# Performance work log

Hardware: AMD Instinct MI355X
Metric: run time of the kernel (lower is better)

Reference implementation:

```python
import jax, jax.numpy as jnp
import numpy as np

H = 0.01      # RK4 step size (parameter.h)
LAM = 1.0     # stage-cost gate penalty
R_COST = 0.1  # scalar control cost R
WMIN, WMAX = -0.01, 0.01  # disturbance range
B, N_STATES, T_STEPS = 8192, 2, 2048

# substituted plant dynamics (parameter.x1_dot / parameter.x2_dot)
def _x1_dot(x1, x2, u):
    return -2.0 * x1 + x2 + u

def _x2_dot(x1, x2, u):
    return x1 - 2.0 * x2 + u

def _rk4_step(x, u):
    # Faithful to RungeKutta.f: k2 == k3 (both evaluated at x2 + h/2)
    x1, x2 = x[0], x[1]
    k1 = jnp.stack([_x1_dot(x1, x2, u), _x2_dot(x1, x2, u)])
    k2 = jnp.stack([_x1_dot(x1, x2 + H / 2, u), _x2_dot(x1, x2 + H / 2, u)])
    k4 = jnp.stack([_x1_dot(x1, x2 + H, u), _x2_dot(x1, x2 + H, u)])
    return x + H * (k1 + 4.0 * k2 + k4) / 6.0  # (k1+2k2+2k3+k4)/6 with k3=k2


def setup_inputs() -> dict:
    key = jax.random.key(0)
    kw, kK, kL, kM, kMo = jax.random.split(key, 5)
    w = jax.random.uniform(kw, (B, N_STATES, T_STEPS), dtype=jnp.float32,
                           minval=WMIN, maxval=WMAX)
    K = 0.1 * jax.random.normal(kK, (1, N_STATES), dtype=jnp.float32)
    L = 0.05 * jax.random.normal(kL, (2 * N_STATES, 2 * N_STATES), dtype=jnp.float32)
    M = 0.05 * jax.random.normal(kM, (1, 2 * N_STATES), dtype=jnp.float32)
    Mo = 0.05 * jax.random.normal(kMo, (1, 1), dtype=jnp.float32)
    return {"w": w, "K": K, "L": L, "M": M, "Mo": Mo}


def reference(w, K, L, M, Mo):
    # w: (B, N, T) disturbances; returns per-sample trajectory cost J, shape (B,)
    Bsz, N, T = w.shape
    dt = w.dtype
    Q = jnp.eye(N, dtype=dt)
    Qf = 10.0 * jnp.eye(N, dtype=dt)
    x0 = jnp.zeros((N,), dtype=dt).at[0].set(1.0)  # xf = 0
    steps = jnp.arange(T)

    def traj_cost(w_b):  # w_b: (N, T)
        def step(carry, inp):
            x, x_hat = carry          # each (N,)
            w_t, i = inp
            z = jnp.concatenate([x, x_hat])            # phi input (2N,)
            phi = z @ L @ z + M[0] @ z + Mo[0, 0]
            delta = jnp.where(i == 0, jnp.asarray(1.0, dt), jax.nn.sigmoid(phi))
            x_hat_n = jnp.where(i == 0, x_hat, delta * x + (1.0 - delta) * x_hat)
            u = K[0] @ x_hat_n                         # control from gated estimate
            x_next = _rk4_step(x, u) + w_t
            u_s = K[0] @ x                             # J uses K @ x[:,i]
            sc = x @ Q @ x + R_COST * u_s * u_s + LAM * delta
            return (x_next, x_hat_n), sc

        (x_T, _), scs = jax.lax.scan(step, (x0, x0), (w_b.T, steps))
        return jnp.sum(scs[: T - 1]) + x_T @ Qf @ x_T

    return jax.vmap(traj_cost)(w)
```

## Files before the change

kernel.cpp:

```cpp
#include <hip/hip_runtime.h>


#define T_STEPS 2048
#define BATCH   8192

__device__ __forceinline__ float swapf(float v) {
    return __int_as_float(__builtin_amdgcn_update_dpp(
        0, __float_as_int(v), 0xB1, 0xF, 0xF, true));
}

__global__ __launch_bounds__(64, 1) void cstr_kernel(
    const float* __restrict__ w,
    const float* __restrict__ K,
    const float* __restrict__ L,
    const float* __restrict__ M,
    const float* __restrict__ Mo,
    float* __restrict__ out)
{
    const int lane = threadIdx.x;
    const int p = lane & 1;
    const int s = blockIdx.x * 32 + (lane >> 1);

    const float k1c = K[0], k2c = K[1];
    const float s11 = L[0];
    const float s12 = L[1] + L[4];
    const float s13 = L[2] + L[8];
    const float s14 = L[3] + L[12];
    const float s22 = L[5];
    const float s23 = L[6] + L[9];
    const float s24 = L[7] + L[13];
    const float s33 = L[10];
    const float s34 = L[11] + L[14];
    const float s44 = L[15];
    const float m1 = M[0], m2 = M[1], m3 = M[2], m4 = M[3];
    const float c0 = Mo[0];

    constexpr float Hs = 0.01f;
    constexpr float Ad = 1.0f - 2.0f * Hs;
    constexpr float RU = 0.1f / (Hs * Hs);
    constexpr float SC = -1.44269504088896340736f;

    float P1, P2, P3, P4, P5, P6, P7, P8;
    if (p == 0) { P1 = s11; P2 = s12; P3 = s13; P4 = s14; P5 = m1; P6 = s33; P7 = s34; P8 = m3; }
    else        { P1 = s22; P2 = 0.f; P3 = s24; P4 = s23; P5 = m2; P6 = s44; P7 = 0.f; P8 = m4; }
    P1 *= SC; P2 *= SC; P3 *= SC; P4 *= SC; P5 *= SC; P6 *= SC; P7 *= SC; P8 *= SC;
    const float P9 = 0.5f * c0 * SC;

    const float hk   = Hs * (p ? k2c : k1c);
    const float Cown = p ? (-Hs * Hs) : (0.5f * Hs * Hs);

    float x  = p ? 0.0f : 1.0f;
    float xh = x;
    float hkxh = Hs * k1c;
    float accO = 0.0f;
    float accU = 0.0f;
    float accD = 0.0f;

    auto step = [&](float wv, bool first, bool cost) {
        float xo  = swapf(x);
        float xho = swapf(xh);
        float hkx_h = hk * x;
        float hkx   = hkx_h + swapf(hkx_h);
        float base  = fmaf(Ad, x, fmaf(Hs, xo, wv + Cown));
        float dxh   = x - xh;
        float dk    = hkx - hkxh;
        if (cost) {
            accO = fmaf(x, x, accO);
            accU = fmaf(hkx, hkx, accU);
        }
        float d;
        if (first) {
            d = 1.0f;
        } else {
            float t  = fmaf(P2, xo, fmaf(P1, x, P5));
            t        = fmaf(P3, xh, t);
            t        = fmaf(P4, xho, t);
            float u2 = fmaf(P7, xho, fmaf(P6, xh, P8));
            float part = fmaf(xh, u2, fmaf(x, t, P9));
            float e  = __builtin_amdgcn_exp2f(part + swapf(part));
            d        = __builtin_amdgcn_rcpf(1.0f + e);
        }
        if (cost) accD += d;
        xh = fmaf(d, dxh, xh);
        float hu = fmaf(d, dk, hkxh);
        hkxh = hu;
        x = base + hu;
    };

    auto chunk = [&](const float4* buf, bool first, bool lastchunk) {
        #pragma unroll
        for (int q = 0; q < 4; ++q) {
            float4 a = buf[q];
            step(a.x, first && (q == 0), true);
            step(a.y, false, true);
            step(a.z, false, true);
            step(a.w, false, !(lastchunk && (q == 3)));
        }
    };

    const float4* r = reinterpret_cast<const float4*>(
        w + ((size_t)s * 2 + p) * T_STEPS);

    float4 Abuf[4], Bbuf[4];
    #pragma unroll
    for (int q = 0; q < 4; ++q) Abuf[q] = r[q];
    #pragma unroll
    for (int q = 0; q < 4; ++q) Bbuf[q] = r[4 + q];

    chunk(Abuf, true, false);

    for (int i = 0; i < 63; ++i) {
        const float4* pa = r + (size_t)(2 + 2 * i) * 4;
        #pragma unroll
        for (int q = 0; q < 4; ++q) Abuf[q] = pa[q];
        chunk(Bbuf, false, false);
        const float4* pb = r + (size_t)(3 + 2 * i) * 4;
        #pragma unroll
        for (int q = 0; q < 4; ++q) Bbuf[q] = pb[q];
        chunk(Abuf, false, false);
    }
    chunk(Bbuf, false, true);

    accO = fmaf(10.0f * x, x, accO);
    float J = accO + swapf(accO) + fmaf(RU, accU, accD);
    if (p == 0) out[s] = J;
}

extern "C" void kernel_launch(void* const* d_in, const int* in_sizes, int n_in,
                              void* d_out, int out_size, void* d_ws, size_t ws_size,
                              hipStream_t stream) {
    const float* w  = (const float*)d_in[0];
    const float* K  = (const float*)d_in[1];
    const float* L  = (const float*)d_in[2];
    const float* M  = (const float*)d_in[3];
    const float* Mo = (const float*)d_in[4];
    float* out = (float*)d_out;

    hipLaunchKernelGGL(cstr_kernel, dim3(BATCH * 2 / 64), dim3(64), 0, stream,
                       w, K, L, M, Mo, out);
}
```

Measured before the change: 303.8 us.

## Interleave two trajectories per thread to expose instruction-level parallelism

```diff
diff --git a/kernel.cpp b/kernel.cpp
--- a/kernel.cpp
+++ b/kernel.cpp
@@ -9,6 +9,10 @@
         0, __float_as_int(v), 0xB1, 0xF, 0xF, true));
 }
 
+struct St {
+    float x, xh, hkxh, accO, accU, accD;
+};
+
 __global__ __launch_bounds__(64, 1) void cstr_kernel(
     const float* __restrict__ w,
     const float* __restrict__ K,
@@ -19,7 +23,9 @@
 {
     const int lane = threadIdx.x;
     const int p = lane & 1;
-    const int s = blockIdx.x * 32 + (lane >> 1);
+    const int j = lane >> 1;
+    const int sA = blockIdx.x * 64 + j;
+    const int sB = sA + 32;
 
     const float k1c = K[0], k2c = K[1];
     const float s11 = L[0];
@@ -49,81 +55,85 @@
     const float hk   = Hs * (p ? k2c : k1c);
     const float Cown = p ? (-Hs * Hs) : (0.5f * Hs * Hs);
 
-    float x  = p ? 0.0f : 1.0f;
-    float xh = x;
-    float hkxh = Hs * k1c;
-    float accO = 0.0f;
-    float accU = 0.0f;
-    float accD = 0.0f;
+    St A, B;
+    A.x = p ? 0.0f : 1.0f;  A.xh = A.x;  A.hkxh = Hs * k1c;
+    A.accO = 0.0f; A.accU = 0.0f; A.accD = 0.0f;
+    B = A;
 
-    auto step = [&](float wv, bool first, bool cost) {
-        float xo  = swapf(x);
-        float xho = swapf(xh);
-        float hkx_h = hk * x;
+    auto step = [&](St& S, float wv, bool first, bool cost) {
+        float xo  = swapf(S.x);
+        float xho = swapf(S.xh);
+        float hkx_h = hk * S.x;
         float hkx   = hkx_h + swapf(hkx_h);
-        float base  = fmaf(Ad, x, fmaf(Hs, xo, wv + Cown));
-        float dxh   = x - xh;
-        float dk    = hkx - hkxh;
+        float base  = fmaf(Ad, S.x, fmaf(Hs, xo, wv + Cown));
+        float dxh   = S.x - S.xh;
+        float dk    = hkx - S.hkxh;
         if (cost) {
-            accO = fmaf(x, x, accO);
-            accU = fmaf(hkx, hkx, accU);
+            S.accO = fmaf(S.x, S.x, S.accO);
+            S.accU = fmaf(hkx, hkx, S.accU);
         }
         float d;
         if (first) {
             d = 1.0f;
         } else {
-            float t  = fmaf(P2, xo, fmaf(P1, x, P5));
-            t        = fmaf(P3, xh, t);
+            float t  = fmaf(P2, xo, fmaf(P1, S.x, P5));
+            t        = fmaf(P3, S.xh, t);
             t        = fmaf(P4, xho, t);
-            float u2 = fmaf(P7, xho, fmaf(P6, xh, P8));
-            float part = fmaf(xh, u2, fmaf(x, t, P9));
+            float u2 = fmaf(P7, xho, fmaf(P6, S.xh, P8));
+            float part = fmaf(S.x, t, fmaf(S.xh, u2, P9));
             float e  = __builtin_amdgcn_exp2f(part + swapf(part));
             d        = __builtin_amdgcn_rcpf(1.0f + e);
         }
-        if (cost) accD += d;
-        xh = fmaf(d, dxh, xh);
-        float hu = fmaf(d, dk, hkxh);
-        hkxh = hu;
-        x = base + hu;
+        if (cost) S.accD += d;
+        S.xh = fmaf(d, dxh, S.xh);
+        float hu = fmaf(d, dk, S.hkxh);
+        S.hkxh = hu;
+        S.x = base + hu;
     };
 
-    auto chunk = [&](const float4* buf, bool first, bool lastchunk) {
+    auto chunk2 = [&](const float4* bA, const float4* bB, bool first, bool lastchunk) {
         #pragma unroll
         for (int q = 0; q < 4; ++q) {
-            float4 a = buf[q];
-            step(a.x, first && (q == 0), true);
-            step(a.y, false, true);
-            step(a.z, false, true);
-            step(a.w, false, !(lastchunk && (q == 3)));
+            float4 a = bA[q], b = bB[q];
+            bool f = first && (q == 0);
+            step(A, a.x, f, true);  step(B, b.x, f, true);
+            step(A, a.y, false, true);  step(B, b.y, false, true);
+            step(A, a.z, false, true);  step(B, b.z, false, true);
+            bool c = !(lastchunk && (q == 3));
+            step(A, a.w, false, c);  step(B, b.w, false, c);
         }
     };
 
-    const float4* r = reinterpret_cast<const float4*>(
-        w + ((size_t)s * 2 + p) * T_STEPS);
+    const float4* rA = reinterpret_cast<const float4*>(w + ((size_t)sA * 2 + p) * T_STEPS);
+    const float4* rB = reinterpret_cast<const float4*>(w + ((size_t)sB * 2 + p) * T_STEPS);
 
-    float4 Abuf[4], Bbuf[4];
+    float4 XA[4], YA[4], XB[4], YB[4];
     #pragma unroll
-    for (int q = 0; q < 4; ++q) Abuf[q] = r[q];
+    for (int q = 0; q < 4; ++q) { XA[q] = rA[q];     XB[q] = rB[q]; }
     #pragma unroll
-    for (int q = 0; q < 4; ++q) Bbuf[q] = r[4 + q];
+    for (int q = 0; q < 4; ++q) { YA[q] = rA[4 + q]; YB[q] = rB[4 + q]; }
 
-    chunk(Abuf, true, false);
+    chunk2(XA, XB, true, false);
 
     for (int i = 0; i < 63; ++i) {
-        const float4* pa = r + (size_t)(2 + 2 * i) * 4;
+        const float4* pa = rA + (size_t)(2 + 2 * i) * 4;
+        const float4* pb = rB + (size_t)(2 + 2 * i) * 4;
         #pragma unroll
-        for (int q = 0; q < 4; ++q) Abuf[q] = pa[q];
-        chunk(Bbuf, false, false);
-        const float4* pb = r + (size_t)(3 + 2 * i) * 4;
+        for (int q = 0; q < 4; ++q) { XA[q] = pa[q]; XB[q] = pb[q]; }
+        chunk2(YA, YB, false, false);
+        const float4* qa = rA + (size_t)(3 + 2 * i) * 4;
+        const float4* qb = rB + (size_t)(3 + 2 * i) * 4;
         #pragma unroll
-        for (int q = 0; q < 4; ++q) Bbuf[q] = pb[q];
-        chunk(Abuf, false, false);
+        for (int q = 0; q < 4; ++q) { YA[q] = qa[q]; YB[q] = qb[q]; }
+        chunk2(XA, XB, false, false);
     }
-    chunk(Bbuf, false, true);
+    chunk2(YA, YB, false, true);
 
-    accO = fmaf(10.0f * x, x, accO);
-    float J = accO + swapf(accO) + fmaf(RU, accU, accD);
-    if (p == 0) out[s] = J;
+    A.accO = fmaf(10.0f * A.x, A.x, A.accO);
+    B.accO = fmaf(10.0f * B.x, B.x, B.accO);
+    float JA = A.accO + swapf(A.accO) + fmaf(RU, A.accU, A.accD);
+    float JB = B.accO + swapf(B.accO) + fmaf(RU, B.accU, B.accD);
+    if (p == 0) { out[sA] = JA; out[sB] = JB; }
 }
 
 extern "C" void kernel_launch(void* const* d_in, const int* in_sizes, int n_in,
@@ -136,6 +146,6 @@
     const float* Mo = (const float*)d_in[4];
     float* out = (float*)d_out;
 
-    hipLaunchKernelGGL(cstr_kernel, dim3(BATCH * 2 / 64), dim3(64), 0, stream,
+    hipLaunchKernelGGL(cstr_kernel, dim3(BATCH / 64), dim3(64), 0, stream,
                        w, K, L, M, Mo, out);
 }
```

After: 456.3 us. 1.5x slower.
